# Performance work log

Hardware: AMD Instinct MI355X
Metric: run time of the kernel (lower is better)

## Reference

```python
import jax, jax.numpy as jnp
import numpy as np

EMB_DIM = 256
HID = (EMB_DIM // 2) * 2   # 256, second Linear in-dim
IN_DIM = (EMB_DIM // 2) * 4  # 512, first Linear in-dim


def setup_inputs() -> dict:
    key = jax.random.key(0)
    k1, k2, k3, k4 = jax.random.split(key, 4)
    N = 512
    x = jax.random.normal(k1, (N, EMB_DIM), dtype=jnp.float32)
    y = jax.random.normal(k2, (N, EMB_DIM), dtype=jnp.float32)
    # MLP params (stored [in, out]); init scale ~ PyTorch Linear default
    s1 = 1.0 / np.sqrt(IN_DIM)
    s2 = 1.0 / np.sqrt(HID)
    W1 = jax.random.uniform(k3, (IN_DIM, HID), dtype=jnp.float32, minval=-s1, maxval=s1)
    b1 = jnp.zeros((HID,), dtype=jnp.float32)
    W2 = jax.random.uniform(k4, (HID, 1), dtype=jnp.float32, minval=-s2, maxval=s2)
    b2 = jnp.zeros((1,), dtype=jnp.float32)
    return {"x_samples": x, "y_samples": y, "W1": W1, "b1": b1, "W2": W2, "b2": b2}


def reference(x_samples, y_samples, W1, b1, W2, b2):
    N = y_samples.shape[0]
    d = x_samples.shape[-1]
    # Split first-layer weight so the [N,N,2d] concat buffer is never built:
    W1x, W1y = W1[:d], W1[d:]

    def head(h):  # second Linear + Softplus; h: [..., HID] -> [..., 1]
        return jax.nn.softplus(h @ W2 + b2)

    # T0: paired scores, [N, 1]
    h0 = jax.nn.relu(x_samples @ W1x + y_samples @ W1y + b1)
    T0 = head(h0)

    # T1: pairwise scores. x_tile[i,j]=x[j], y_tile[i,j]=y[i] -> [N, N, 1]
    hx = x_samples @ W1x  # [N, HID] (j index)
    hy = y_samples @ W1y  # [N, HID] (i index)
    h1 = jax.nn.relu(hy[:, None, :] + hx[None, :, :] + b1)  # [N, N, HID]
    T1 = head(h1)  # [N, N, 1]

    lse = jax.nn.logsumexp(T1, axis=1)  # [N, 1]
    lower_bound = T0.mean() - (lse.mean() - jnp.log(jnp.float32(N)))
    return -lower_bound
```

## Files before the change

### kernel.cpp

```cpp
#include <hip/hip_runtime.h>
#include <math.h>

#define NN 512
#define D  256
#define MAGIC1 0x5EC7A9B1
#define MAGIC2 0x3D8F6C25

__device__ __forceinline__ void store64_sys(void* p, float a, float b) {
    union { float f[2]; unsigned long long u; } v;
    v.f[0] = a; v.f[1] = b;
    __hip_atomic_store((unsigned long long*)p, v.u, __ATOMIC_RELAXED, __HIP_MEMORY_SCOPE_SYSTEM);
}
__device__ __forceinline__ void store32_sys(float* p, float a) {
    __hip_atomic_store(p, a, __ATOMIC_RELAXED, __HIP_MEMORY_SCOPE_SYSTEM);
}

__global__ __launch_bounds__(512) void fused(
    const float* __restrict__ x, const float* __restrict__ y,
    const float* __restrict__ W1, const float* __restrict__ b1,
    const float* __restrict__ W2, const float* __restrict__ b2p,
    float* __restrict__ hxbT, float* __restrict__ hy,
    float* __restrict__ partials, int* __restrict__ flag1, int* __restrict__ flag2,
    float* __restrict__ out)
{
    int b = blockIdx.x;
    int tid = threadIdx.x;

    {
        bool isx = (b < 128);
        int r0 = (b & 127) * 4 + (tid >> 8) * 2;
        int k  = tid & 255;
        const float* src = isx ? x : y;
        const float* Wb  = W1 + (isx ? 0 : D * D);

        float bias = isx ? b1[k] : 0.0f;
        float a0 = bias, a1 = bias;

        const float4* s0 = (const float4*)(src + (r0 + 0) * D);
        const float4* s1 = (const float4*)(src + (r0 + 1) * D);

#pragma unroll 4
        for (int m4 = 0; m4 < D / 4; ++m4) {
            float4 v0 = s0[m4], v1 = s1[m4];
            const float* Wc = Wb + (m4 * 4) * D + k;
            float w0 = Wc[0], w1 = Wc[D], w2 = Wc[2 * D], w3 = Wc[3 * D];
            a0 = fmaf(v0.x, w0, a0); a0 = fmaf(v0.y, w1, a0);
            a0 = fmaf(v0.z, w2, a0); a0 = fmaf(v0.w, w3, a0);
            a1 = fmaf(v1.x, w0, a1); a1 = fmaf(v1.y, w1, a1);
            a1 = fmaf(v1.z, w2, a1); a1 = fmaf(v1.w, w3, a1);
        }

        if (isx) {
            store64_sys(hxbT + k * NN + r0, a0, a1);
        } else {
            store32_sys(&hy[(r0 + 0) * D + k], a0);
            store32_sys(&hy[(r0 + 1) * D + k], a1);
        }
    }

    __syncthreads();
    if (tid == 0)
        __hip_atomic_store(&flag1[b], MAGIC1, __ATOMIC_RELAXED, __HIP_MEMORY_SCOPE_SYSTEM);

    if (tid < 256) {
        while (__hip_atomic_load(&flag1[tid], __ATOMIC_RELAXED, __HIP_MEMORY_SCOPE_SYSTEM) != MAGIC1)
            __builtin_amdgcn_s_sleep(2);
    }
    __syncthreads();
    if (tid < 64)
        __builtin_amdgcn_fence(__ATOMIC_ACQUIRE, "agent");
    __syncthreads();

    __shared__ float hyS[2][D];
    __shared__ float w2S[D];
    __shared__ float zS[4][2][NN];
    __shared__ float ws0[8], ws1[8], diagS[2];

    int i0 = b * 2;
    if (tid < 256) {
        hyS[0][tid] = hy[(i0 + 0) * D + tid];
        w2S[tid]    = W2[tid];
    } else {
        int u = tid - 256;
        hyS[1][u] = hy[(i0 + 1) * D + u];
    }
    __syncthreads();

    int jg = tid & 127;
    int ks = tid >> 7;

    float p00 = 0.f, p01 = 0.f, p02 = 0.f, p03 = 0.f;
    float p10 = 0.f, p11 = 0.f, p12 = 0.f, p13 = 0.f;

    const float4* hT   = (const float4*)hxbT;
    const float4* hy0f = (const float4*)hyS[0];
    const float4* hy1f = (const float4*)hyS[1];
    const float4* w2f  = (const float4*)w2S;
    int g0 = ks * 16;

#pragma unroll 2
    for (int g = 0; g < 16; ++g) {
        int k4 = g0 + g;
        float4 a4 = hy0f[k4];
        float4 c4 = hy1f[k4];
        float4 w4 = w2f[k4];
        float4 h0 = hT[(k4 * 4 + 0) * (NN / 4) + jg];
        float4 h1 = hT[(k4 * 4 + 1) * (NN / 4) + jg];
        float4 h2 = hT[(k4 * 4 + 2) * (NN / 4) + jg];
        float4 h3 = hT[(k4 * 4 + 3) * (NN / 4) + jg];

        p00 = fmaf(fmaxf(h0.x + a4.x, 0.f), w4.x, p00);
        p01 = fmaf(fmaxf(h0.y + a4.x, 0.f), w4.x, p01);
        p02 = fmaf(fmaxf(h0.z + a4.x, 0.f), w4.x, p02);
        p03 = fmaf(fmaxf(h0.w + a4.x, 0.f), w4.x, p03);
        p10 = fmaf(fmaxf(h0.x + c4.x, 0.f), w4.x, p10);
        p11 = fmaf(fmaxf(h0.y + c4.x, 0.f), w4.x, p11);
        p12 = fmaf(fmaxf(h0.z + c4.x, 0.f), w4.x, p12);
        p13 = fmaf(fmaxf(h0.w + c4.x, 0.f), w4.x, p13);

        p00 = fmaf(fmaxf(h1.x + a4.y, 0.f), w4.y, p00);
        p01 = fmaf(fmaxf(h1.y + a4.y, 0.f), w4.y, p01);
        p02 = fmaf(fmaxf(h1.z + a4.y, 0.f), w4.y, p02);
        p03 = fmaf(fmaxf(h1.w + a4.y, 0.f), w4.y, p03);
        p10 = fmaf(fmaxf(h1.x + c4.y, 0.f), w4.y, p10);
        p11 = fmaf(fmaxf(h1.y + c4.y, 0.f), w4.y, p11);
        p12 = fmaf(fmaxf(h1.z + c4.y, 0.f), w4.y, p12);
        p13 = fmaf(fmaxf(h1.w + c4.y, 0.f), w4.y, p13);

        p00 = fmaf(fmaxf(h2.x + a4.z, 0.f), w4.z, p00);
        p01 = fmaf(fmaxf(h2.y + a4.z, 0.f), w4.z, p01);
        p02 = fmaf(fmaxf(h2.z + a4.z, 0.f), w4.z, p02);
        p03 = fmaf(fmaxf(h2.w + a4.z, 0.f), w4.z, p03);
        p10 = fmaf(fmaxf(h2.x + c4.z, 0.f), w4.z, p10);
        p11 = fmaf(fmaxf(h2.y + c4.z, 0.f), w4.z, p11);
        p12 = fmaf(fmaxf(h2.z + c4.z, 0.f), w4.z, p12);
        p13 = fmaf(fmaxf(h2.w + c4.z, 0.f), w4.z, p13);

        p00 = fmaf(fmaxf(h3.x + a4.w, 0.f), w4.w, p00);
        p01 = fmaf(fmaxf(h3.y + a4.w, 0.f), w4.w, p01);
        p02 = fmaf(fmaxf(h3.z + a4.w, 0.f), w4.w, p02);
        p03 = fmaf(fmaxf(h3.w + a4.w, 0.f), w4.w, p03);
        p10 = fmaf(fmaxf(h3.x + c4.w, 0.f), w4.w, p10);
        p11 = fmaf(fmaxf(h3.y + c4.w, 0.f), w4.w, p11);
        p12 = fmaf(fmaxf(h3.z + c4.w, 0.f), w4.w, p12);
        p13 = fmaf(fmaxf(h3.w + c4.w, 0.f), w4.w, p13);
    }

    *(float4*)&zS[ks][0][4 * jg] = make_float4(p00, p01, p02, p03);
    *(float4*)&zS[ks][1][4 * jg] = make_float4(p10, p11, p12, p13);
    __syncthreads();

    float b2 = b2p[0];
    float z0 = zS[0][0][tid] + zS[1][0][tid] + zS[2][0][tid] + zS[3][0][tid] + b2;
    float z1 = zS[0][1][tid] + zS[1][1][tid] + zS[2][1][tid] + zS[3][1][tid] + b2;
    float e0 = expf(z0), e1 = expf(z1);

    int lane = tid & 63, wid = tid >> 6;
    if (tid == i0)     diagS[0] = fmaxf(z0, 0.f) + log1pf(expf(-fabsf(z0)));
    if (tid == i0 + 1) diagS[1] = fmaxf(z1, 0.f) + log1pf(expf(-fabsf(z1)));

    float s0 = e0, s1 = e1;
#pragma unroll
    for (int off = 32; off >= 1; off >>= 1) {
        s0 += __shfl_xor(s0, off);
        s1 += __shfl_xor(s1, off);
    }
    if (lane == 0) { ws0[wid] = s0; ws1[wid] = s1; }
    __syncthreads();

    if (tid == 0) {
        float tot0 = 512.0f, tot1 = 512.0f;
#pragma unroll
        for (int w = 0; w < 8; ++w) { tot0 += ws0[w]; tot1 += ws1[w]; }
        float lse0 = logf(tot0), lse1 = logf(tot1);
        float part = (lse0 - diagS[0] + lse1 - diagS[1]) * (1.0f / 512.0f);
        if (b == 0) part -= logf(512.0f);
        store32_sys(&partials[b], part);
        asm volatile("s_waitcnt vmcnt(0)" ::: "memory");
        __hip_atomic_store(&flag2[b], MAGIC2, __ATOMIC_RELAXED, __HIP_MEMORY_SCOPE_SYSTEM);
    }

    if (b == 0) {
        if (tid < 256) {
            while (__hip_atomic_load(&flag2[tid], __ATOMIC_RELAXED, __HIP_MEMORY_SCOPE_SYSTEM) != MAGIC2)
                __builtin_amdgcn_s_sleep(2);
        }
        __syncthreads();
        if (tid < 64) {
            float s = 0.0f;
#pragma unroll
            for (int q = 0; q < 4; ++q)
                s += __hip_atomic_load(&partials[tid + 64 * q], __ATOMIC_RELAXED, __HIP_MEMORY_SCOPE_SYSTEM);
#pragma unroll
            for (int off = 32; off >= 1; off >>= 1) s += __shfl_xor(s, off);
            if (tid == 0) out[0] = s;
        }
    }
}

extern "C" void kernel_launch(void* const* d_in, const int* in_sizes, int n_in,
                              void* d_out, int out_size, void* d_ws, size_t ws_size,
                              hipStream_t stream)
{
    const float* x  = (const float*)d_in[0];
    const float* y  = (const float*)d_in[1];
    const float* W1 = (const float*)d_in[2];
    const float* b1 = (const float*)d_in[3];
    const float* W2 = (const float*)d_in[4];
    const float* b2 = (const float*)d_in[5];
    float* out = (float*)d_out;

    float* ws   = (float*)d_ws;
    float* hxbT = ws;
    float* hy   = ws + NN * D;
    float* partials = ws + 2 * NN * D;
    int* flag1 = (int*)(ws + 2 * NN * D + 256);
    int* flag2 = (int*)(ws + 2 * NN * D + 512);

    fused<<<256, 512, 0, stream>>>(x, y, W1, b1, W2, b2,
                                   hxbT, hy, partials, flag1, flag2, out);
}
```

Measured before the change: 31.77 us.

## Keep hy rows in LDS, wait only on producer flags, issue cache-bypass vector loads

Each block now computes both its own two hx rows and the two hy rows it later consumes, so hy goes straight into shared memory and no longer round-trips through global memory. The grid-wide barrier on all 256 flags is replaced by each thread spinning only on the two flags for the hx columns it reads. The pairwise loop now uses inline-asm global_load_dwordx4 with sc0 sc1 cache bits, eight loads in flight per batch. This removes one global write/read phase and shortens the barrier wait, at the cost of the acquire fence, relying instead on the cache-bypass loads for visibility.

```diff
diff --git a/kernel.cpp b/kernel.cpp
--- a/kernel.cpp
+++ b/kernel.cpp
@@ -6,10 +6,13 @@
 #define MAGIC1 0x5EC7A9B1
 #define MAGIC2 0x3D8F6C25
 
+typedef unsigned long long u64;
+typedef float f32x4 __attribute__((ext_vector_type(4)));
+
 __device__ __forceinline__ void store64_sys(void* p, float a, float b) {
-    union { float f[2]; unsigned long long u; } v;
+    union { float f[2]; u64 u; } v;
     v.f[0] = a; v.f[1] = b;
-    __hip_atomic_store((unsigned long long*)p, v.u, __ATOMIC_RELAXED, __HIP_MEMORY_SCOPE_SYSTEM);
+    __hip_atomic_store((u64*)p, v.u, __ATOMIC_RELAXED, __HIP_MEMORY_SCOPE_SYSTEM);
 }
 __device__ __forceinline__ void store32_sys(float* p, float a) {
     __hip_atomic_store(p, a, __ATOMIC_RELAXED, __HIP_MEMORY_SCOPE_SYSTEM);
@@ -19,21 +22,25 @@
     const float* __restrict__ x, const float* __restrict__ y,
     const float* __restrict__ W1, const float* __restrict__ b1,
     const float* __restrict__ W2, const float* __restrict__ b2p,
-    float* __restrict__ hxbT, float* __restrict__ hy,
+    float* __restrict__ hxbT,
     float* __restrict__ partials, int* __restrict__ flag1, int* __restrict__ flag2,
     float* __restrict__ out)
 {
     int b = blockIdx.x;
     int tid = threadIdx.x;
 
+    __shared__ float hyS[2][D];
+    __shared__ float w2S[D];
+    __shared__ float zS[4][2][NN];
+    __shared__ float ws0[8], ws1[8], diagS[2];
+
     {
-        bool isx = (b < 128);
-        int r0 = (b & 127) * 4 + (tid >> 8) * 2;
-        int k  = tid & 255;
-        const float* src = isx ? x : y;
-        const float* Wb  = W1 + (isx ? 0 : D * D);
-
-        float bias = isx ? b1[k] : 0.0f;
+        int half = tid >> 8;
+        int col  = tid & 255;
+        int r0   = 2 * b;
+        const float* src = half ? y : x;
+        const float* Wb  = W1 + half * (D * D);
+        float bias = half ? 0.0f : b1[col];
         float a0 = bias, a1 = bias;
 
         const float4* s0 = (const float4*)(src + (r0 + 0) * D);
@@ -42,7 +49,7 @@
 #pragma unroll 4
         for (int m4 = 0; m4 < D / 4; ++m4) {
             float4 v0 = s0[m4], v1 = s1[m4];
-            const float* Wc = Wb + (m4 * 4) * D + k;
+            const float* Wc = Wb + (m4 * 4) * D + col;
             float w0 = Wc[0], w1 = Wc[D], w2 = Wc[2 * D], w3 = Wc[3 * D];
             a0 = fmaf(v0.x, w0, a0); a0 = fmaf(v0.y, w1, a0);
             a0 = fmaf(v0.z, w2, a0); a0 = fmaf(v0.w, w3, a0);
@@ -50,11 +57,12 @@
             a1 = fmaf(v1.z, w2, a1); a1 = fmaf(v1.w, w3, a1);
         }
 
-        if (isx) {
-            store64_sys(hxbT + k * NN + r0, a0, a1);
+        if (half == 0) {
+            store64_sys(hxbT + col * NN + r0, a0, a1);
         } else {
-            store32_sys(&hy[(r0 + 0) * D + k], a0);
-            store32_sys(&hy[(r0 + 1) * D + k], a1);
+            hyS[0][col] = a0;
+            hyS[1][col] = a1;
+            w2S[col]    = W2[col];
         }
     }
 
@@ -62,95 +70,62 @@
     if (tid == 0)
         __hip_atomic_store(&flag1[b], MAGIC1, __ATOMIC_RELAXED, __HIP_MEMORY_SCOPE_SYSTEM);
 
-    if (tid < 256) {
-        while (__hip_atomic_load(&flag1[tid], __ATOMIC_RELAXED, __HIP_MEMORY_SCOPE_SYSTEM) != MAGIC1)
-            __builtin_amdgcn_s_sleep(2);
-    }
-    __syncthreads();
-    if (tid < 64)
-        __builtin_amdgcn_fence(__ATOMIC_ACQUIRE, "agent");
-    __syncthreads();
-
-    __shared__ float hyS[2][D];
-    __shared__ float w2S[D];
-    __shared__ float zS[4][2][NN];
-    __shared__ float ws0[8], ws1[8], diagS[2];
-
-    int i0 = b * 2;
-    if (tid < 256) {
-        hyS[0][tid] = hy[(i0 + 0) * D + tid];
-        w2S[tid]    = W2[tid];
-    } else {
-        int u = tid - 256;
-        hyS[1][u] = hy[(i0 + 1) * D + u];
-    }
-    __syncthreads();
-
     int jg = tid & 127;
     int ks = tid >> 7;
 
-    float p00 = 0.f, p01 = 0.f, p02 = 0.f, p03 = 0.f;
-    float p10 = 0.f, p11 = 0.f, p12 = 0.f, p13 = 0.f;
+    while (__hip_atomic_load(&flag1[2 * jg], __ATOMIC_RELAXED, __HIP_MEMORY_SCOPE_SYSTEM) != MAGIC1)
+        __builtin_amdgcn_s_sleep(2);
+    while (__hip_atomic_load(&flag1[2 * jg + 1], __ATOMIC_RELAXED, __HIP_MEMORY_SCOPE_SYSTEM) != MAGIC1)
+        __builtin_amdgcn_s_sleep(2);
 
-    const float4* hT   = (const float4*)hxbT;
-    const float4* hy0f = (const float4*)hyS[0];
-    const float4* hy1f = (const float4*)hyS[1];
-    const float4* w2f  = (const float4*)w2S;
-    int g0 = ks * 16;
+    f32x4 p0 = {0.f, 0.f, 0.f, 0.f};
+    f32x4 p1 = {0.f, 0.f, 0.f, 0.f};
+    unsigned vbase = (unsigned)(ks * 64 * (NN * 4) + jg * 16);
 
-#pragma unroll 2
-    for (int g = 0; g < 16; ++g) {
-        int k4 = g0 + g;
-        float4 a4 = hy0f[k4];
-        float4 c4 = hy1f[k4];
-        float4 w4 = w2f[k4];
-        float4 h0 = hT[(k4 * 4 + 0) * (NN / 4) + jg];
-        float4 h1 = hT[(k4 * 4 + 1) * (NN / 4) + jg];
-        float4 h2 = hT[(k4 * 4 + 2) * (NN / 4) + jg];
-        float4 h3 = hT[(k4 * 4 + 3) * (NN / 4) + jg];
+#pragma unroll
+    for (int c = 0; c < 8; ++c) {
+        f32x4 h[8];
+#pragma unroll
+        for (int q = 0; q < 8; ++q) {
+            unsigned vo = vbase + (unsigned)((c * 8 + q) * (NN * 4));
+            asm volatile("global_load_dwordx4 %0, %1, %2 sc0 sc1"
+                         : "=v"(h[q]) : "v"(vo), "s"(hxbT) : "memory");
+        }
+        asm volatile("s_waitcnt vmcnt(0)" ::: "memory");
+        __builtin_amdgcn_sched_barrier(0);
 
-        p00 = fmaf(fmaxf(h0.x + a4.x, 0.f), w4.x, p00);
-        p01 = fmaf(fmaxf(h0.y + a4.x, 0.f), w4.x, p01);
-        p02 = fmaf(fmaxf(h0.z + a4.x, 0.f), w4.x, p02);
-        p03 = fmaf(fmaxf(h0.w + a4.x, 0.f), w4.x, p03);
-        p10 = fmaf(fmaxf(h0.x + c4.x, 0.f), w4.x, p10);
-        p11 = fmaf(fmaxf(h0.y + c4.x, 0.f), w4.x, p11);
-        p12 = fmaf(fmaxf(h0.z + c4.x, 0.f), w4.x, p12);
-        p13 = fmaf(fmaxf(h0.w + c4.x, 0.f), w4.x, p13);
+        int k0 = ks * 64 + c * 8;
+        f32x4 aA = *(const f32x4*)&hyS[0][k0];
+        f32x4 aB = *(const f32x4*)&hyS[0][k0 + 4];
+        f32x4 cA = *(const f32x4*)&hyS[1][k0];
+        f32x4 cB = *(const f32x4*)&hyS[1][k0 + 4];
+        f32x4 wA = *(const f32x4*)&w2S[k0];
+        f32x4 wB = *(const f32x4*)&w2S[k0 + 4];
+        float av[8] = {aA[0], aA[1], aA[2], aA[3], aB[0], aB[1], aB[2], aB[3]};
+        float cv[8] = {cA[0], cA[1], cA[2], cA[3], cB[0], cB[1], cB[2], cB[3]};
+        float wv[8] = {wA[0], wA[1], wA[2], wA[3], wB[0], wB[1], wB[2], wB[3]};
 
-        p00 = fmaf(fmaxf(h1.x + a4.y, 0.f), w4.y, p00);
-        p01 = fmaf(fmaxf(h1.y + a4.y, 0.f), w4.y, p01);
-        p02 = fmaf(fmaxf(h1.z + a4.y, 0.f), w4.y, p02);
-        p03 = fmaf(fmaxf(h1.w + a4.y, 0.f), w4.y, p03);
-        p10 = fmaf(fmaxf(h1.x + c4.y, 0.f), w4.y, p10);
-        p11 = fmaf(fmaxf(h1.y + c4.y, 0.f), w4.y, p11);
-        p12 = fmaf(fmaxf(h1.z + c4.y, 0.f), w4.y, p12);
-        p13 = fmaf(fmaxf(h1.w + c4.y, 0.f), w4.y, p13);
-
-        p00 = fmaf(fmaxf(h2.x + a4.z, 0.f), w4.z, p00);
-        p01 = fmaf(fmaxf(h2.y + a4.z, 0.f), w4.z, p01);
-        p02 = fmaf(fmaxf(h2.z + a4.z, 0.f), w4.z, p02);
-        p03 = fmaf(fmaxf(h2.w + a4.z, 0.f), w4.z, p03);
-        p10 = fmaf(fmaxf(h2.x + c4.z, 0.f), w4.z, p10);
-        p11 = fmaf(fmaxf(h2.y + c4.z, 0.f), w4.z, p11);
-        p12 = fmaf(fmaxf(h2.z + c4.z, 0.f), w4.z, p12);
-        p13 = fmaf(fmaxf(h2.w + c4.z, 0.f), w4.z, p13);
-
-        p00 = fmaf(fmaxf(h3.x + a4.w, 0.f), w4.w, p00);
-        p01 = fmaf(fmaxf(h3.y + a4.w, 0.f), w4.w, p01);
-        p02 = fmaf(fmaxf(h3.z + a4.w, 0.f), w4.w, p02);
-        p03 = fmaf(fmaxf(h3.w + a4.w, 0.f), w4.w, p03);
-        p10 = fmaf(fmaxf(h3.x + c4.w, 0.f), w4.w, p10);
-        p11 = fmaf(fmaxf(h3.y + c4.w, 0.f), w4.w, p11);
-        p12 = fmaf(fmaxf(h3.z + c4.w, 0.f), w4.w, p12);
-        p13 = fmaf(fmaxf(h3.w + c4.w, 0.f), w4.w, p13);
+#pragma unroll
+        for (int e = 0; e < 8; ++e) {
+            f32x4 hv = h[e];
+            float a = av[e], cc = cv[e], w = wv[e];
+            p0[0] = fmaf(fmaxf(hv[0] + a, 0.f), w, p0[0]);
+            p0[1] = fmaf(fmaxf(hv[1] + a, 0.f), w, p0[1]);
+            p0[2] = fmaf(fmaxf(hv[2] + a, 0.f), w, p0[2]);
+            p0[3] = fmaf(fmaxf(hv[3] + a, 0.f), w, p0[3]);
+            p1[0] = fmaf(fmaxf(hv[0] + cc, 0.f), w, p1[0]);
+            p1[1] = fmaf(fmaxf(hv[1] + cc, 0.f), w, p1[1]);
+            p1[2] = fmaf(fmaxf(hv[2] + cc, 0.f), w, p1[2]);
+            p1[3] = fmaf(fmaxf(hv[3] + cc, 0.f), w, p1[3]);
+        }
     }
 
-    *(float4*)&zS[ks][0][4 * jg] = make_float4(p00, p01, p02, p03);
-    *(float4*)&zS[ks][1][4 * jg] = make_float4(p10, p11, p12, p13);
+    *(f32x4*)&zS[ks][0][4 * jg] = p0;
+    *(f32x4*)&zS[ks][1][4 * jg] = p1;
     __syncthreads();
 
     float b2 = b2p[0];
+    int i0 = 2 * b;
     float z0 = zS[0][0][tid] + zS[1][0][tid] + zS[2][0][tid] + zS[3][0][tid] + b2;
     float z1 = zS[0][1][tid] + zS[1][1][tid] + zS[2][1][tid] + zS[3][1][tid] + b2;
     float e0 = expf(z0), e1 = expf(z1);
@@ -212,11 +187,10 @@
 
     float* ws   = (float*)d_ws;
     float* hxbT = ws;
-    float* hy   = ws + NN * D;
-    float* partials = ws + 2 * NN * D;
-    int* flag1 = (int*)(ws + 2 * NN * D + 256);
-    int* flag2 = (int*)(ws + 2 * NN * D + 512);
+    float* partials = ws + NN * D;
+    int* flag1 = (int*)(ws + NN * D + 256);
+    int* flag2 = flag1 + 256;
 
     fused<<<256, 512, 0, stream>>>(x, y, W1, b1, W2, b2,
-                                   hxbT, hy, partials, flag1, flag2, out);
+                                   hxbT, partials, flag1, flag2, out);
 }
```

Result: slower. 103.3 us (+225.2%).

## Compute each block's own hy rows locally in shared memory instead of via global

Applied to the files above, without the earlier changes.

Each block now computes the x-projection for its two rows (written to global for all blocks) and the y-projection for the same two rows, which it keeps directly in shared memory. This removes the global hy buffer, its system-scope stores and the reload after the grid barrier, and shrinks the pre-barrier work split. The spin-wait sleep interval is also raised, which cuts polling traffic but may add latency before waiting blocks notice the flag.

```diff
diff --git a/kernel.cpp b/kernel.cpp
--- a/kernel.cpp
+++ b/kernel.cpp
@@ -6,10 +6,12 @@
 #define MAGIC1 0x5EC7A9B1
 #define MAGIC2 0x3D8F6C25
 
+typedef unsigned long long u64;
+
 __device__ __forceinline__ void store64_sys(void* p, float a, float b) {
-    union { float f[2]; unsigned long long u; } v;
+    union { float f[2]; u64 u; } v;
     v.f[0] = a; v.f[1] = b;
-    __hip_atomic_store((unsigned long long*)p, v.u, __ATOMIC_RELAXED, __HIP_MEMORY_SCOPE_SYSTEM);
+    __hip_atomic_store((u64*)p, v.u, __ATOMIC_RELAXED, __HIP_MEMORY_SCOPE_SYSTEM);
 }
 __device__ __forceinline__ void store32_sys(float* p, float a) {
     __hip_atomic_store(p, a, __ATOMIC_RELAXED, __HIP_MEMORY_SCOPE_SYSTEM);
@@ -19,21 +21,25 @@
     const float* __restrict__ x, const float* __restrict__ y,
     const float* __restrict__ W1, const float* __restrict__ b1,
     const float* __restrict__ W2, const float* __restrict__ b2p,
-    float* __restrict__ hxbT, float* __restrict__ hy,
+    float* __restrict__ hxbT,
     float* __restrict__ partials, int* __restrict__ flag1, int* __restrict__ flag2,
     float* __restrict__ out)
 {
     int b = blockIdx.x;
     int tid = threadIdx.x;
 
+    __shared__ float hyS[2][D];
+    __shared__ float w2S[D];
+    __shared__ float zS[4][2][NN];
+    __shared__ float ws0[8], ws1[8], diagS[2];
+
     {
-        bool isx = (b < 128);
-        int r0 = (b & 127) * 4 + (tid >> 8) * 2;
-        int k  = tid & 255;
-        const float* src = isx ? x : y;
-        const float* Wb  = W1 + (isx ? 0 : D * D);
-
-        float bias = isx ? b1[k] : 0.0f;
+        int half = tid >> 8;
+        int col  = tid & 255;
+        int r0   = 2 * b;
+        const float* src = half ? y : x;
+        const float* Wb  = W1 + half * (D * D);
+        float bias = half ? 0.0f : b1[col];
         float a0 = bias, a1 = bias;
 
         const float4* s0 = (const float4*)(src + (r0 + 0) * D);
@@ -42,7 +48,7 @@
 #pragma unroll 4
         for (int m4 = 0; m4 < D / 4; ++m4) {
             float4 v0 = s0[m4], v1 = s1[m4];
-            const float* Wc = Wb + (m4 * 4) * D + k;
+            const float* Wc = Wb + (m4 * 4) * D + col;
             float w0 = Wc[0], w1 = Wc[D], w2 = Wc[2 * D], w3 = Wc[3 * D];
             a0 = fmaf(v0.x, w0, a0); a0 = fmaf(v0.y, w1, a0);
             a0 = fmaf(v0.z, w2, a0); a0 = fmaf(v0.w, w3, a0);
@@ -50,11 +56,12 @@
             a1 = fmaf(v1.z, w2, a1); a1 = fmaf(v1.w, w3, a1);
         }
 
-        if (isx) {
-            store64_sys(hxbT + k * NN + r0, a0, a1);
+        if (half == 0) {
+            store64_sys(hxbT + col * NN + r0, a0, a1);
         } else {
-            store32_sys(&hy[(r0 + 0) * D + k], a0);
-            store32_sys(&hy[(r0 + 1) * D + k], a1);
+            hyS[0][col] = a0;
+            hyS[1][col] = a1;
+            w2S[col]    = W2[col];
         }
     }
 
@@ -64,26 +71,11 @@
 
     if (tid < 256) {
         while (__hip_atomic_load(&flag1[tid], __ATOMIC_RELAXED, __HIP_MEMORY_SCOPE_SYSTEM) != MAGIC1)
-            __builtin_amdgcn_s_sleep(2);
+            __builtin_amdgcn_s_sleep(16);
     }
     __syncthreads();
     if (tid < 64)
         __builtin_amdgcn_fence(__ATOMIC_ACQUIRE, "agent");
-    __syncthreads();
-
-    __shared__ float hyS[2][D];
-    __shared__ float w2S[D];
-    __shared__ float zS[4][2][NN];
-    __shared__ float ws0[8], ws1[8], diagS[2];
-
-    int i0 = b * 2;
-    if (tid < 256) {
-        hyS[0][tid] = hy[(i0 + 0) * D + tid];
-        w2S[tid]    = W2[tid];
-    } else {
-        int u = tid - 256;
-        hyS[1][u] = hy[(i0 + 1) * D + u];
-    }
     __syncthreads();
 
     int jg = tid & 127;
@@ -151,6 +143,7 @@
     __syncthreads();
 
     float b2 = b2p[0];
+    int i0 = 2 * b;
     float z0 = zS[0][0][tid] + zS[1][0][tid] + zS[2][0][tid] + zS[3][0][tid] + b2;
     float z1 = zS[0][1][tid] + zS[1][1][tid] + zS[2][1][tid] + zS[3][1][tid] + b2;
     float e0 = expf(z0), e1 = expf(z1);
@@ -183,7 +176,7 @@
     if (b == 0) {
         if (tid < 256) {
             while (__hip_atomic_load(&flag2[tid], __ATOMIC_RELAXED, __HIP_MEMORY_SCOPE_SYSTEM) != MAGIC2)
-                __builtin_amdgcn_s_sleep(2);
+                __builtin_amdgcn_s_sleep(16);
         }
         __syncthreads();
         if (tid < 64) {
@@ -212,11 +205,10 @@
 
     float* ws   = (float*)d_ws;
     float* hxbT = ws;
-    float* hy   = ws + NN * D;
-    float* partials = ws + 2 * NN * D;
-    int* flag1 = (int*)(ws + 2 * NN * D + 256);
-    int* flag2 = (int*)(ws + 2 * NN * D + 512);
+    float* partials = ws + NN * D;
+    int* flag1 = (int*)(ws + NN * D + 256);
+    int* flag2 = flag1 + 256;
 
     fused<<<256, 512, 0, stream>>>(x, y, W1, b1, W2, b2,
-                                   hxbT, hy, partials, flag1, flag2, out);
-}
+                                   hxbT, partials, flag1, flag2, out);
+}
```

New measurement: 31.13 us. 1.02x faster.
